# Kernel optimization log

Hardware: AMD Instinct MI355X
Metric: run time of the kernel (lower is better)

## Reference

```python
import jax, jax.numpy as jnp
import numpy as np

W_RESIDUAL = 0.5  # cfg.MODEL.TRM.RESIDUAL weight
EPS = 1e-12      # F.normalize eps


def _l2norm(x, axis):
    n = jnp.sqrt(jnp.sum(x * x, axis=axis, keepdims=True))
    return x / jnp.maximum(n, EPS)


def setup_inputs() -> dict:
    key = jax.random.key(0)
    k1, k2, k3, k4 = jax.random.split(key, 4)
    B, NS, NP, C, T = 32, 16, 8, 256, 128
    return {
        "map2d_iou": jax.random.normal(k1, (B, C, T, T), dtype=jnp.float32),
        "sent_feat": jax.random.normal(k2, (B, NS, C), dtype=jnp.float32),
        "phrase_feat": jax.random.normal(k3, (B, NS, NP, C), dtype=jnp.float32),
        "phrase_weight": jax.random.uniform(k4, (B, NS, NP), dtype=jnp.float32),
        "phrase_mask": jnp.ones((B, NS, NP), dtype=jnp.float32),
    }


def reference(map2d_iou, sent_feat, phrase_feat, phrase_weight, phrase_mask):
    B, C, T, _ = map2d_iou.shape
    NS, NP = phrase_feat.shape[1], phrase_feat.shape[2]
    # valid 2D proposals: start <= end (upper triangular)
    mask2d = jnp.triu(jnp.ones((T, T), dtype=map2d_iou.dtype))

    # F.normalize(vid_feat_iou, dim=0) per video, flattened to (B, C, T*T)
    vid_norm = _l2norm(map2d_iou, axis=1).reshape(B, C, T * T)

    # phrase scores: normalize each phrase feat over C, mm with video map
    ph_norm = _l2norm(phrase_feat, axis=-1)                       # B,NS,NP,C
    ph_scores = jnp.einsum("bspc,bcm->bspm", ph_norm, vid_norm)   # B,NS,NP,T*T
    phrase_score_map = (jax.nn.sigmoid(ph_scores * 10.0).reshape(B, NS, NP, T, T)
                        * mask2d * phrase_mask[:, :, :, None, None])

    # phrase-weighted aggregation: (B,NS,1,NP) @ (B,NS,NP,T*T)
    ph_att = jnp.einsum("bsp,bspm->bsm", phrase_weight, ph_scores).reshape(B, NS, T, T)

    # sentence scores
    sf_norm = _l2norm(sent_feat, axis=-1)                         # B,NS,C
    sf_scores = jnp.einsum("bsc,bcm->bsm", sf_norm, vid_norm).reshape(B, NS, T, T)

    iou_scores = jax.nn.sigmoid((sf_scores + W_RESIDUAL * ph_att) * 10.0) * mask2d
    return iou_scores, phrase_score_map
```

## Files before the change

kernel.cpp:

```cpp
#include <hip/hip_runtime.h>
#include <hip/hip_bf16.h>

#define B_   32
#define NS_  16
#define NP_  8
#define C_   256
#define T_   128
#define M_   (T_*T_)
#define NF_  144
#define MT_  128
#define KC_  32
#define NCH_ (C_/KC_)

typedef __attribute__((ext_vector_type(4))) float f32x4;
typedef __attribute__((ext_vector_type(8))) short s16x8;
typedef __attribute__((ext_vector_type(4))) short s16x4;
typedef __attribute__((ext_vector_type(4))) int   i32x4;
typedef __attribute__((ext_vector_type(2))) int   i32x2;

#define KSTR 20
#define SUBT 644
#define VBUF 5152
#define ABUF_DW 2304

#define LDS_BYTES 39040
#define AB_OFF    20608

__device__ __forceinline__ short f2bf(float f) {
  unsigned u = __builtin_bit_cast(unsigned, f);
  u += 0x7fffu + ((u >> 16) & 1u);
  return (short)(u >> 16);
}
__device__ __forceinline__ int cvt_pk_bf16(float a, float b) {
  int d;
  asm("v_cvt_pk_bf16_f32 %0, %1, %2" : "=v"(d) : "v"(a), "v"(b));
  return d;
}
__device__ __forceinline__ float sigm(float z) { return 1.0f / (1.0f + __expf(-z)); }

__global__ void prep_feats(const float* __restrict__ sf, const float* __restrict__ pf,
                           short* __restrict__ Fb) {
  const int bs = blockIdx.x;
  const int b  = bs >> 4, s = bs & 15;
  const int t  = threadIdx.x;
  __shared__ float red[4];
  const int kc   = t >> 5;
  const int kk   = t & 31;
  const int half = kk >> 4;
  const int g    = (kk & 15) >> 2;
  const int j    = kk & 3;
  const int pos  = 8 * g + 4 * half + j;
  for (int v = 0; v < 9; ++v) {
    float x = (v < 8) ? pf[(((size_t)bs) * NP_ + v) * C_ + t]
                      : sf[((size_t)bs) * C_ + t];
    float ss = x * x;
    #pragma unroll
    for (int off = 32; off; off >>= 1) ss += __shfl_xor(ss, off);
    __syncthreads();
    if ((t & 63) == 0) red[t >> 6] = ss;
    __syncthreads();
    const float tot = red[0] + red[1] + red[2] + red[3];
    const float rn = 1.0f / fmaxf(sqrtf(tot), 1e-12f);
    const int row = (v < 8) ? (s * NP_ + v) : (128 + s);
    Fb[(((size_t)(b * 8 + kc)) * NF_ + row) * 32 + pos] = f2bf(x * rn);
  }
}

__global__ void __launch_bounds__(512, 6) trm_main(
    const float* __restrict__ V,
    const int* __restrict__ FbD,
    const float* __restrict__ pw,
    const float* __restrict__ pm,
    float* __restrict__ out0,
    float* __restrict__ out1) {
  __shared__ __align__(16) char smem[LDS_BYTES];
  short* vb  = (short*)smem;
  int*   abI = (int*)(smem + AB_OFF);
  short* abS = (short*)(smem + AB_OFF);
  float* pbuf = (float*)(smem + AB_OFF);
  float* rnl  = (float*)(smem + AB_OFF + 8192);
  float* att  = (float*)(smem + AB_OFF + 8704);
  float* pwl  = (float*)(smem + AB_OFF + 17152);
  float* pml  = (float*)(smem + AB_OFF + 17664);

  const int tid  = threadIdx.x;
  const int b    = blockIdx.y;
  const int tile = blockIdx.x;
  const int m0   = tile * MT_;

  const int c4 = tid & 31;
  const int rg = tid >> 5;
  const size_t vbase = ((size_t)b * C_) * M_ + m0 + c4 * 4;
  const int smt  = c4 >> 2;
  const int scc0 = (c4 & 3) * 4;

  const int lane = tid & 63;
  const int w  = tid >> 6;
  const int g  = lane >> 4;
  const int cc = lane & 15;

  f32x4 acc[9];
  #pragma unroll
  for (int i = 0; i < 9; ++i) acc[i] = (f32x4){0.f, 0.f, 0.f, 0.f};

  float4 r[2];
  i32x4 a0;
  int a2;
  float ssq0 = 0.f, ssq1 = 0.f, ssq2 = 0.f, ssq3 = 0.f;

  const int* AbBase = FbD + (size_t)b * 8 * ABUF_DW;

  r[0] = *(const float4*)(V + vbase + (size_t)rg * M_);
  r[1] = *(const float4*)(V + vbase + (size_t)(rg + 16) * M_);
  a0 = *(const i32x4*)(AbBase + tid * 4);
  a2 = AbBase[2048 + (tid & 255)];
  #pragma unroll
  for (int i = 0; i < 2; ++i) {
    const int kk = rg + i * 16;
    ssq0 += r[i].x * r[i].x; ssq1 += r[i].y * r[i].y;
    ssq2 += r[i].z * r[i].z; ssq3 += r[i].w * r[i].w;
    i32x2 pk = {cvt_pk_bf16(r[i].x, r[i].y), cvt_pk_bf16(r[i].z, r[i].w)};
    *(i32x2*)(&vb[smt * SUBT + kk * KSTR + scc0]) = pk;
  }
  {
    int* Ad = abI;
    *(i32x4*)(Ad + tid * 4) = a0;
    if (tid < 256) Ad[2048 + tid] = a2;
  }
  __syncthreads();

  int cur = 0;
  for (int kc = 0; kc < NCH_; ++kc) {
    if (kc < NCH_ - 1) {
      r[0] = *(const float4*)(V + vbase + (size_t)((kc + 1) * KC_ + rg) * M_);
      r[1] = *(const float4*)(V + vbase + (size_t)((kc + 1) * KC_ + rg + 16) * M_);
      const int* Ab = AbBase + (kc + 1) * ABUF_DW;
      a0 = *(const i32x4*)(Ab + tid * 4);
      a2 = Ab[2048 + (tid & 255)];
    }
    {
      s16x8 bf;
      const int base = cur * VBUF + w * SUBT + cc;
      #pragma unroll
      for (int j = 0; j < 4; ++j) {
        bf[j]     = vb[base + (4 * g + j) * KSTR];
        bf[j + 4] = vb[base + (16 + 4 * g + j) * KSTR];
      }
      const short* Arow = abS + cur * (ABUF_DW * 2) + cc * 32 + g * 8;
      #pragma unroll
      for (int ft = 0; ft < 9; ++ft) {
        const s16x8 af = *(const s16x8*)(Arow + ft * (16 * 32));
        acc[ft] = __builtin_amdgcn_mfma_f32_16x16x32_bf16(af, bf, acc[ft], 0, 0, 0);
      }
    }
    if (kc < NCH_ - 1) {
      #pragma unroll
      for (int i = 0; i < 2; ++i) {
        const int kk = rg + i * 16;
        ssq0 += r[i].x * r[i].x; ssq1 += r[i].y * r[i].y;
        ssq2 += r[i].z * r[i].z; ssq3 += r[i].w * r[i].w;
        i32x2 pk = {cvt_pk_bf16(r[i].x, r[i].y), cvt_pk_bf16(r[i].z, r[i].w)};
        *(i32x2*)(&vb[(cur ^ 1) * VBUF + smt * SUBT + kk * KSTR + scc0]) = pk;
      }
      int* Ad = abI + (cur ^ 1) * ABUF_DW;
      *(i32x4*)(Ad + tid * 4) = a0;
      if (tid < 256) Ad[2048 + tid] = a2;
      __syncthreads();
      cur ^= 1;
    }
  }

  __syncthreads();

  {
    f32x4 p = {ssq0, ssq1, ssq2, ssq3};
    *(f32x4*)(&pbuf[rg * 128 + c4 * 4]) = p;
  }
  if (tid < 128) { pwl[tid] = pw[b * 128 + tid]; pml[tid] = pm[b * 128 + tid]; }
  __syncthreads();
  if (tid < 128) {
    float ss = 0.f;
    #pragma unroll
    for (int qq = 0; qq < 16; ++qq) ss += pbuf[qq * 128 + tid];
    rnl[tid] = 1.0f / fmaxf(sqrtf(ss), 1e-12f);
  }
  __syncthreads();

  {
    const int col = w * 16 + cc;
    const float rn = rnl[col];
    const int m = m0 + col;
    const float msk = (col >= tile) ? 1.0f : 0.0f;
    #pragma unroll
    for (int ft = 0; ft < 8; ++ft) {
      float pa = 0.f;
      #pragma unroll
      for (int rr = 0; rr < 4; ++rr) {
        const int f = ft * 16 + 4 * g + rr;
        const float raw = acc[ft][rr] * rn;
        out1[(((size_t)(b * NS_ + (f >> 3)) * NP_ + (f & 7)) << 14) + m] =
            sigm(10.0f * raw) * msk * pml[f];
        pa += pwl[f] * raw;
      }
      pa += __shfl_xor(pa, 16);
      if ((g & 1) == 0) att[(2 * ft + (g >> 1)) * 132 + col] = pa;
    }
  }
  __syncthreads();
  {
    const int col = w * 16 + cc;
    const float rn = rnl[col];
    const int m = m0 + col;
    const float msk = (col >= tile) ? 1.0f : 0.0f;
    #pragma unroll
    for (int rr = 0; rr < 4; ++rr) {
      const int s = 4 * g + rr;
      const float sfv = acc[8][rr] * rn;
      const float pa = att[s * 132 + col];
      out0[(((size_t)(b * NS_ + s)) << 14) + m] = sigm(10.0f * (sfv + 0.5f * pa)) * msk;
    }
  }
}

extern "C" void kernel_launch(void* const* d_in, const int* in_sizes, int n_in,
                              void* d_out, int out_size, void* d_ws, size_t ws_size,
                              hipStream_t stream) {
  const float* V  = (const float*)d_in[0];
  const float* sf = (const float*)d_in[1];
  const float* pf = (const float*)d_in[2];
  const float* pw = (const float*)d_in[3];
  const float* pm = (const float*)d_in[4];
  float* out0 = (float*)d_out;
  float* out1 = out0 + (size_t)B_ * NS_ * M_;
  short* Fb = (short*)d_ws;

  prep_feats<<<B_ * NS_, 256, 0, stream>>>(sf, pf, Fb);
  dim3 grid(M_ / MT_, B_);
  trm_main<<<grid, 512, 0, stream>>>(V, (const int*)Fb, pw, pm, out0, out1);
}
```

Before: 279.3 us.

## Drop LDS staging: load V and feature fragments directly into MFMA registers

The main kernel no longer stages the video map and normalized features through double-buffered shared memory. Each lane loads its MFMA operand elements straight from global memory, with register prefetch of the next chunk, and reduces column norms via shuffles. The tile shrinks to 64 columns with 256 threads, and outputs use nontemporal stores. This removes LDS traffic and barriers, but global loads become narrower and feature fragments are re-read from cache by every block.

```diff
diff --git a/kernel.cpp b/kernel.cpp
--- a/kernel.cpp
+++ b/kernel.cpp
@@ -8,23 +8,14 @@
 #define T_   128
 #define M_   (T_*T_)
 #define NF_  144
-#define MT_  128
+#define MT_  64
 #define KC_  32
 #define NCH_ (C_/KC_)
+#define ABUF_DW 2304
 
 typedef __attribute__((ext_vector_type(4))) float f32x4;
 typedef __attribute__((ext_vector_type(8))) short s16x8;
-typedef __attribute__((ext_vector_type(4))) short s16x4;
 typedef __attribute__((ext_vector_type(4))) int   i32x4;
-typedef __attribute__((ext_vector_type(2))) int   i32x2;
-
-#define KSTR 20
-#define SUBT 644
-#define VBUF 5152
-#define ABUF_DW 2304
-
-#define LDS_BYTES 39040
-#define AB_OFF    20608
 
 __device__ __forceinline__ short f2bf(float f) {
   unsigned u = __builtin_bit_cast(unsigned, f);
@@ -66,159 +57,109 @@
   }
 }
 
-__global__ void __launch_bounds__(512, 6) trm_main(
+__global__ void __launch_bounds__(256, 4) trm_main(
     const float* __restrict__ V,
     const int* __restrict__ FbD,
     const float* __restrict__ pw,
     const float* __restrict__ pm,
     float* __restrict__ out0,
     float* __restrict__ out1) {
-  __shared__ __align__(16) char smem[LDS_BYTES];
-  short* vb  = (short*)smem;
-  int*   abI = (int*)(smem + AB_OFF);
-  short* abS = (short*)(smem + AB_OFF);
-  float* pbuf = (float*)(smem + AB_OFF);
-  float* rnl  = (float*)(smem + AB_OFF + 8192);
-  float* att  = (float*)(smem + AB_OFF + 8704);
-  float* pwl  = (float*)(smem + AB_OFF + 17152);
-  float* pml  = (float*)(smem + AB_OFF + 17664);
+  __shared__ float pwl[128];
+  __shared__ float pml[128];
+  __shared__ float att[16 * 68];
 
   const int tid  = threadIdx.x;
   const int b    = blockIdx.y;
   const int tile = blockIdx.x;
   const int m0   = tile * MT_;
 
-  const int c4 = tid & 31;
-  const int rg = tid >> 5;
-  const size_t vbase = ((size_t)b * C_) * M_ + m0 + c4 * 4;
-  const int smt  = c4 >> 2;
-  const int scc0 = (c4 & 3) * 4;
+  const int lane = tid & 63;
+  const int w    = tid >> 6;
+  const int g    = lane >> 4;
+  const int cc   = lane & 15;
+  const int col  = w * 16 + cc;
+  const int m    = m0 + col;
 
-  const int lane = tid & 63;
-  const int w  = tid >> 6;
-  const int g  = lane >> 4;
-  const int cc = lane & 15;
+  if (tid < 128) { pwl[tid] = pw[b * 128 + tid]; pml[tid] = pm[b * 128 + tid]; }
+
+  const float* Vb = V + (size_t)b * C_ * M_ + m;
+  const int*   Ab = FbD + (size_t)b * 8 * ABUF_DW + cc * 16 + g * 4;
 
   f32x4 acc[9];
   #pragma unroll
   for (int i = 0; i < 9; ++i) acc[i] = (f32x4){0.f, 0.f, 0.f, 0.f};
 
-  float4 r[2];
-  i32x4 a0;
-  int a2;
-  float ssq0 = 0.f, ssq1 = 0.f, ssq2 = 0.f, ssq3 = 0.f;
+  float ssq = 0.f;
+  float c0[8], c1[8];
+  const int kb0 = 4 * g;
 
-  const int* AbBase = FbD + (size_t)b * 8 * ABUF_DW;
+  #pragma unroll
+  for (int j = 0; j < 4; ++j) {
+    c0[j]     = Vb[(size_t)(kb0 + j) * M_];
+    c0[j + 4] = Vb[(size_t)(16 + kb0 + j) * M_];
+  }
 
-  r[0] = *(const float4*)(V + vbase + (size_t)rg * M_);
-  r[1] = *(const float4*)(V + vbase + (size_t)(rg + 16) * M_);
-  a0 = *(const i32x4*)(AbBase + tid * 4);
-  a2 = AbBase[2048 + (tid & 255)];
   #pragma unroll
-  for (int i = 0; i < 2; ++i) {
-    const int kk = rg + i * 16;
-    ssq0 += r[i].x * r[i].x; ssq1 += r[i].y * r[i].y;
-    ssq2 += r[i].z * r[i].z; ssq3 += r[i].w * r[i].w;
-    i32x2 pk = {cvt_pk_bf16(r[i].x, r[i].y), cvt_pk_bf16(r[i].z, r[i].w)};
-    *(i32x2*)(&vb[smt * SUBT + kk * KSTR + scc0]) = pk;
-  }
-  {
-    int* Ad = abI;
-    *(i32x4*)(Ad + tid * 4) = a0;
-    if (tid < 256) Ad[2048 + tid] = a2;
-  }
-  __syncthreads();
-
-  int cur = 0;
   for (int kc = 0; kc < NCH_; ++kc) {
     if (kc < NCH_ - 1) {
-      r[0] = *(const float4*)(V + vbase + (size_t)((kc + 1) * KC_ + rg) * M_);
-      r[1] = *(const float4*)(V + vbase + (size_t)((kc + 1) * KC_ + rg + 16) * M_);
-      const int* Ab = AbBase + (kc + 1) * ABUF_DW;
-      a0 = *(const i32x4*)(Ab + tid * 4);
-      a2 = Ab[2048 + (tid & 255)];
-    }
-    {
-      s16x8 bf;
-      const int base = cur * VBUF + w * SUBT + cc;
+      const int kb = (kc + 1) * KC_ + kb0;
       #pragma unroll
       for (int j = 0; j < 4; ++j) {
-        bf[j]     = vb[base + (4 * g + j) * KSTR];
-        bf[j + 4] = vb[base + (16 + 4 * g + j) * KSTR];
-      }
-      const short* Arow = abS + cur * (ABUF_DW * 2) + cc * 32 + g * 8;
-      #pragma unroll
-      for (int ft = 0; ft < 9; ++ft) {
-        const s16x8 af = *(const s16x8*)(Arow + ft * (16 * 32));
-        acc[ft] = __builtin_amdgcn_mfma_f32_16x16x32_bf16(af, bf, acc[ft], 0, 0, 0);
+        c1[j]     = Vb[(size_t)(kb + j) * M_];
+        c1[j + 4] = Vb[(size_t)(16 + kb + j) * M_];
       }
     }
-    if (kc < NCH_ - 1) {
-      #pragma unroll
-      for (int i = 0; i < 2; ++i) {
-        const int kk = rg + i * 16;
-        ssq0 += r[i].x * r[i].x; ssq1 += r[i].y * r[i].y;
-        ssq2 += r[i].z * r[i].z; ssq3 += r[i].w * r[i].w;
-        i32x2 pk = {cvt_pk_bf16(r[i].x, r[i].y), cvt_pk_bf16(r[i].z, r[i].w)};
-        *(i32x2*)(&vb[(cur ^ 1) * VBUF + smt * SUBT + kk * KSTR + scc0]) = pk;
-      }
-      int* Ad = abI + (cur ^ 1) * ABUF_DW;
-      *(i32x4*)(Ad + tid * 4) = a0;
-      if (tid < 256) Ad[2048 + tid] = a2;
-      __syncthreads();
-      cur ^= 1;
+    #pragma unroll
+    for (int j = 0; j < 8; ++j) ssq += c0[j] * c0[j];
+    i32x4 pk;
+    pk[0] = cvt_pk_bf16(c0[0], c0[1]);
+    pk[1] = cvt_pk_bf16(c0[2], c0[3]);
+    pk[2] = cvt_pk_bf16(c0[4], c0[5]);
+    pk[3] = cvt_pk_bf16(c0[6], c0[7]);
+    const s16x8 bf = __builtin_bit_cast(s16x8, pk);
+    const int* Ak = Ab + kc * ABUF_DW;
+    #pragma unroll
+    for (int ft = 0; ft < 9; ++ft) {
+      const i32x4 aw = *(const i32x4*)(Ak + ft * 256);
+      const s16x8 af = __builtin_bit_cast(s16x8, aw);
+      acc[ft] = __builtin_amdgcn_mfma_f32_16x16x32_bf16(af, bf, acc[ft], 0, 0, 0);
     }
+    #pragma unroll
+    for (int j = 0; j < 8; ++j) c0[j] = c1[j];
   }
+
+  ssq += __shfl_xor(ssq, 16);
+  ssq += __shfl_xor(ssq, 32);
+  const float rn = 1.0f / fmaxf(sqrtf(ssq), 1e-12f);
 
   __syncthreads();
 
-  {
-    f32x4 p = {ssq0, ssq1, ssq2, ssq3};
-    *(f32x4*)(&pbuf[rg * 128 + c4 * 4]) = p;
-  }
-  if (tid < 128) { pwl[tid] = pw[b * 128 + tid]; pml[tid] = pm[b * 128 + tid]; }
-  __syncthreads();
-  if (tid < 128) {
-    float ss = 0.f;
+  const int   t1  = m >> 7;
+  const float msk = ((m & 127) >= t1) ? 1.0f : 0.0f;
+  const size_t o1base = ((size_t)b * (NS_ * NP_)) << 14;
+
+  #pragma unroll
+  for (int ft = 0; ft < 8; ++ft) {
+    float pa = 0.f;
     #pragma unroll
-    for (int qq = 0; qq < 16; ++qq) ss += pbuf[qq * 128 + tid];
-    rnl[tid] = 1.0f / fmaxf(sqrtf(ss), 1e-12f);
+    for (int rr = 0; rr < 4; ++rr) {
+      const int f = ft * 16 + 4 * g + rr;
+      const float raw = acc[ft][rr] * rn;
+      __builtin_nontemporal_store(sigm(10.0f * raw) * msk * pml[f],
+                                  &out1[o1base + ((size_t)f << 14) + m]);
+      pa += pwl[f] * raw;
+    }
+    pa += __shfl_xor(pa, 16);
+    if ((g & 1) == 0) att[(2 * ft + (g >> 1)) * 68 + col] = pa;
   }
   __syncthreads();
-
-  {
-    const int col = w * 16 + cc;
-    const float rn = rnl[col];
-    const int m = m0 + col;
-    const float msk = (col >= tile) ? 1.0f : 0.0f;
-    #pragma unroll
-    for (int ft = 0; ft < 8; ++ft) {
-      float pa = 0.f;
-      #pragma unroll
-      for (int rr = 0; rr < 4; ++rr) {
-        const int f = ft * 16 + 4 * g + rr;
-        const float raw = acc[ft][rr] * rn;
-        out1[(((size_t)(b * NS_ + (f >> 3)) * NP_ + (f & 7)) << 14) + m] =
-            sigm(10.0f * raw) * msk * pml[f];
-        pa += pwl[f] * raw;
-      }
-      pa += __shfl_xor(pa, 16);
-      if ((g & 1) == 0) att[(2 * ft + (g >> 1)) * 132 + col] = pa;
-    }
-  }
-  __syncthreads();
-  {
-    const int col = w * 16 + cc;
-    const float rn = rnl[col];
-    const int m = m0 + col;
-    const float msk = (col >= tile) ? 1.0f : 0.0f;
-    #pragma unroll
-    for (int rr = 0; rr < 4; ++rr) {
-      const int s = 4 * g + rr;
-      const float sfv = acc[8][rr] * rn;
-      const float pa = att[s * 132 + col];
-      out0[(((size_t)(b * NS_ + s)) << 14) + m] = sigm(10.0f * (sfv + 0.5f * pa)) * msk;
-    }
+  #pragma unroll
+  for (int rr = 0; rr < 4; ++rr) {
+    const int s = 4 * g + rr;
+    const float sfv = acc[8][rr] * rn;
+    const float pa = att[s * 68 + col];
+    __builtin_nontemporal_store(sigm(10.0f * (sfv + 0.5f * pa)) * msk,
+                                &out0[(((size_t)(b * NS_ + s)) << 14) + m]);
   }
 }
 
@@ -236,5 +177,5 @@
 
   prep_feats<<<B_ * NS_, 256, 0, stream>>>(sf, pf, Fb);
   dim3 grid(M_ / MT_, B_);
-  trm_main<<<grid, 512, 0, stream>>>(V, (const int*)Fb, pw, pm, out0, out1);
+  trm_main<<<grid, 256, 0, stream>>>(V, (const int*)Fb, pw, pm, out0, out1);
 }
```

Result: slower. 293.5 us (+5.1%).
